# Kernel optimization log

Hardware: AMD Instinct MI355X
Metric: run time of the kernel (lower is better)

Reference implementation:

```python
import jax, jax.numpy as jnp
import numpy as np

B, H, W, C = 32, 56, 56, 256
HEADS, WS, SS, MLP = 8, 7, 3, 1024
N = WS * WS          # tokens per window = 49
HD = C // HEADS      # head dim = 32
SCALE = HD ** -0.5
EPS = 1e-5


def _rel_pos_index():
    coords = np.stack(np.meshgrid(np.arange(WS), np.arange(WS), indexing='ij')).reshape(2, -1)
    rel = (coords[:, :, None] - coords[:, None, :]).transpose(1, 2, 0)
    rel[:, :, 0] += WS - 1
    rel[:, :, 1] += WS - 1
    rel[:, :, 0] *= 2 * WS - 1
    return rel.sum(-1)  # (49, 49) int


def _shift_mask():
    ma = np.zeros((H, W), np.float32)
    sl = (slice(0, -WS), slice(-WS, -SS), slice(-SS, None))
    cnt = 0
    for hs in sl:
        for ws_ in sl:
            ma[hs, ws_] = cnt
            cnt += 1
    mw = ma.reshape(H // WS, WS, W // WS, WS).transpose(0, 2, 1, 3).reshape(-1, N)
    diff = mw[:, None, :] - mw[:, :, None]
    return np.where(diff != 0, np.float32(-100.0), np.float32(0.0))  # (nW, 49, 49)


_RPI = _rel_pos_index()
_MASK = jnp.asarray(_shift_mask())


def _ln(x, g, b):
    mu = jnp.mean(x, -1, keepdims=True)
    var = jnp.mean(jnp.square(x - mu), -1, keepdims=True)
    return (x - mu) * jax.lax.rsqrt(var + EPS) * g + b


def setup_inputs() -> dict:
    key = jax.random.key(0)
    ks = jax.random.split(key, 6)
    s = 0.02
    return {
        'x': jax.random.normal(ks[0], (B, H * W, C), jnp.float32),
        'qkv_w': jax.random.normal(ks[1], (C, 3 * C), jnp.float32) * s,
        'qkv_b': jnp.zeros((3 * C,), jnp.float32),
        'proj_w': jax.random.normal(ks[2], (C, C), jnp.float32) * s,
        'proj_b': jnp.zeros((C,), jnp.float32),
        'rel_bias': jax.random.normal(ks[3], ((2 * WS - 1) ** 2, HEADS), jnp.float32) * s,
        'ln1_g': jnp.ones((C,), jnp.float32),
        'ln1_b': jnp.zeros((C,), jnp.float32),
        'ln2_g': jnp.ones((C,), jnp.float32),
        'ln2_b': jnp.zeros((C,), jnp.float32),
        'mlp_w1': jax.random.normal(ks[4], (C, MLP), jnp.float32) * s,
        'mlp_b1': jnp.zeros((MLP,), jnp.float32),
        'mlp_w2': jax.random.normal(ks[5], (MLP, C), jnp.float32) * s,
        'mlp_b2': jnp.zeros((C,), jnp.float32),
    }


def reference(x, qkv_w, qkv_b, proj_w, proj_b, rel_bias,
              ln1_g, ln1_b, ln2_g, ln2_b, mlp_w1, mlp_b1, mlp_w2, mlp_b2):
    b = x.shape[0]
    nW = (H // WS) * (W // WS)

    x_skip = x
    xn = _ln(x, ln1_g, ln1_b).reshape(b, H, W, C)
    shifted = jnp.roll(xn, (-SS, -SS), axis=(1, 2))
    # window partition -> (b*nW, N, C)
    xw = shifted.reshape(b, H // WS, WS, W // WS, WS, C)
    xw = xw.transpose(0, 1, 3, 2, 4, 5).reshape(-1, N, C)

    qkv = (xw @ qkv_w + qkv_b).reshape(-1, N, 3, HEADS, HD).transpose(2, 0, 3, 1, 4)
    q, k, v = qkv[0] * SCALE, qkv[1], qkv[2]  # (b*nW, heads, N, hd)

    attn = jnp.einsum('bhnd,bhmd->bhnm', q, k)
    bias = rel_bias[_RPI.reshape(-1)].reshape(N, N, HEADS).transpose(2, 0, 1)
    attn = attn + bias[None]
    attn = attn.reshape(b, nW, HEADS, N, N) + _MASK[None, :, None]
    attn = jax.nn.softmax(attn.reshape(-1, HEADS, N, N), axis=-1)

    out = jnp.einsum('bhnm,bhmd->bhnd', attn, v)
    out = out.transpose(0, 2, 1, 3).reshape(-1, N, C)
    out = out @ proj_w + proj_b

    # window reverse -> (b, H, W, C)
    out = out.reshape(b, H // WS, W // WS, WS, WS, C)
    out = out.transpose(0, 1, 3, 2, 4, 5).reshape(b, H, W, C)
    out = jnp.roll(out, (SS, SS), axis=(1, 2)).reshape(b, H * W, C)

    x = x_skip + out
    x_skip2 = x
    xn2 = _ln(x, ln2_g, ln2_b)
    h = jax.nn.gelu(xn2 @ mlp_w1 + mlp_b1, approximate=False)
    h = h @ mlp_w2 + mlp_b2
    return x_skip2 + h
```

## Files before the change

### kernel.cpp

```cpp
#include <hip/hip_runtime.h>


typedef unsigned short u16;
typedef __attribute__((ext_vector_type(8))) short bfrag8;
typedef __attribute__((ext_vector_type(8))) unsigned short u16x8;
typedef __attribute__((ext_vector_type(4))) float f32x4;

#define WS_TOK 49
#define C_DIM 256
#define M_ROWS 100352
#define N_WIN 2048
#define SCALE_Q 0.17677669529663689f

#if defined(__has_builtin)
#  if __has_builtin(__builtin_amdgcn_global_load_lds)
#    define HAVE_GLL 1
#  endif
#endif
#ifndef HAVE_GLL
#  define HAVE_GLL 0
#endif

__device__ __forceinline__ float u2f(u16 u) {
    union { unsigned int i; float f; } c; c.i = ((unsigned int)u) << 16; return c.f;
}
__device__ __forceinline__ u16 f2u(float f) {
    union { float f; unsigned int i; } c; c.f = f;
    unsigned int i = c.i;
    return (u16)((i + 0x7fffu + ((i >> 16) & 1u)) >> 16);
}
__device__ __forceinline__ int regionOf(int h) {
    return h < 49 ? 0 : (h < 53 ? 1 : 2);
}
__device__ __forceinline__ float gelu_tanh(float v) {
    const float y = 0.79788456080286536f * (v + 0.044715f * v * v * v);
    const float e = __expf(2.f * y);
    const float t = 1.f - 2.f / (e + 1.f);
    return 0.5f * v * (1.f + t);
}

__device__ __forceinline__ void g2l16(const u16* g, u16* l) {
#if HAVE_GLL
    __builtin_amdgcn_global_load_lds((const __attribute__((address_space(1))) void*)g,
                                     (__attribute__((address_space(3))) void*)l, 16, 0, 0);
#else
    *(bfrag8*)l = *(const bfrag8*)g;
#endif
}

__global__ void transpose_k(const float* __restrict__ in, u16* __restrict__ out,
                            int R, int Ccols) {
    int i = blockIdx.x * 256 + threadIdx.x;
    if (i < R * Ccols) {
        int r = i / Ccols, c = i - r * Ccols;
        out[(size_t)c * R + r] = f2u(in[i]);
    }
}

__global__ __launch_bounds__(256) void ln_kernel(const float* __restrict__ xin,
                                                 const float* __restrict__ g,
                                                 const float* __restrict__ b,
                                                 u16* __restrict__ out, int mode) {
    const int w = threadIdx.x >> 6, lane = threadIdx.x & 63;
    const int r = blockIdx.x * 4 + w;
    int s = r;
    if (mode == 0) {
        const int win = r / WS_TOK, tok = r - win * WS_TOK;
        const int b_ = win >> 6, w64 = win & 63;
        const int wr = w64 >> 3, wc = w64 & 7;
        const int th = tok / 7, tw = tok - th * 7;
        int hh = wr * 7 + th + 3; if (hh >= 56) hh -= 56;
        int ww = wc * 7 + tw + 3; if (ww >= 56) ww -= 56;
        s = b_ * 3136 + hh * 56 + ww;
    }
    const float4 u = *(const float4*)(xin + (size_t)s * C_DIM + lane * 4);
    float f0 = u.x, f1 = u.y, f2 = u.z, f3 = u.w;
    float s1 = f0 + f1 + f2 + f3;
    float s2 = f0 * f0 + f1 * f1 + f2 * f2 + f3 * f3;
#pragma unroll
    for (int off = 32; off; off >>= 1) {
        s1 += __shfl_xor(s1, off, 64);
        s2 += __shfl_xor(s2, off, 64);
    }
    const float mu = s1 * (1.f / 256.f);
    const float rs = rsqrtf(s2 * (1.f / 256.f) - mu * mu + 1e-5f);
    const float4 ug = *(const float4*)(g + lane * 4);
    const float4 ub = *(const float4*)(b + lane * 4);
    ushort4 o;
    o.x = f2u((f0 - mu) * rs * ug.x + ub.x);
    o.y = f2u((f1 - mu) * rs * ug.y + ub.y);
    o.z = f2u((f2 - mu) * rs * ug.z + ub.z);
    o.w = f2u((f3 - mu) * rs * ug.w + ub.w);
    *(ushort4*)(out + (size_t)r * C_DIM + lane * 4) = o;
}

template <int KD, int ND, int NY, int EPI>
__global__ __launch_bounds__(256) void gemm_bt(const u16* __restrict__ A,
                                               const u16* __restrict__ Bt,
                                               const float* __restrict__ bias,
                                               u16* __restrict__ o0,
                                               u16* __restrict__ o1,
                                               u16* __restrict__ o2,
                                               float* __restrict__ fo,
                                               const float* __restrict__ res) {
    __shared__ __align__(16) char pool[17408];
    u16* As = (u16*)pool;
    u16* Bs = (u16*)(pool + 8192);
    const int tid = threadIdx.x;
    const int bid = blockIdx.x;
    const int m0 = (bid / NY) * 128;
    const int n0 = (bid % NY) * 128;
    const int wid = tid >> 6, lane = tid & 63;
    const int wy = wid >> 1, wx = wid & 1;
    const int l15 = lane & 15, lsel = lane >> 4;

    f32x4 acc[4][4] = {};
    const u16* Ag = A + (size_t)m0 * KD;
    const u16* Bg = Bt + (size_t)n0 * KD;

    for (int k0 = 0; k0 < KD; k0 += 32) {
#pragma unroll
        for (int p = 0; p < 2; ++p) {
            const int idx = p * 256 + tid;
            const int row = idx >> 2, ks = (idx & 3) << 3;
            g2l16(Ag + (size_t)row * KD + k0 + ks, As + idx * 8);
            g2l16(Bg + (size_t)row * KD + k0 + ks, Bs + idx * 8);
        }
        __syncthreads();
        bfrag8 af[4], bfv[4];
#pragma unroll
        for (int m = 0; m < 4; ++m)
            af[m] = *(const bfrag8*)(As + (wy * 64 + m * 16 + l15) * 32 + lsel * 8);
#pragma unroll
        for (int n = 0; n < 4; ++n)
            bfv[n] = *(const bfrag8*)(Bs + (wx * 64 + n * 16 + l15) * 32 + lsel * 8);
#pragma unroll
        for (int m = 0; m < 4; ++m)
#pragma unroll
            for (int n = 0; n < 4; ++n)
                acc[m][n] = __builtin_amdgcn_mfma_f32_16x16x32_bf16(af[m], bfv[n],
                                                                    acc[m][n], 0, 0, 0);
        __syncthreads();
    }

    float* Ts = (float*)pool + wid * (16 * 68);
    const int r  = lane >> 2;
    const int cg = (lane & 3) << 4;

#pragma unroll
    for (int m = 0; m < 4; ++m) {
#pragma unroll
        for (int n = 0; n < 4; ++n)
#pragma unroll
            for (int reg = 0; reg < 4; ++reg)
                Ts[(lsel * 4 + reg) * 68 + n * 16 + l15] = acc[m][n][reg];
        float vals[16];
#pragma unroll
        for (int j = 0; j < 4; ++j)
            *(f32x4*)(vals + 4 * j) = *(const f32x4*)(Ts + r * 68 + cg + 4 * j);

        const int gr  = m0 + wy * 64 + m * 16 + r;
        const int gc0 = n0 + wx * 64 + cg;
        float bias16[16];
#pragma unroll
        for (int j = 0; j < 4; ++j)
            *(f32x4*)(bias16 + 4 * j) = *(const f32x4*)(bias + gc0 + 4 * j);

        if (EPI == 0) {
            const int win = gr / WS_TOK, tok = gr - win * WS_TOK;
            const int part = gc0 >> 8, head = (gc0 >> 5) & 7, hd = gc0 & 31;
            u16* dst = (part == 0) ? o0 : (part == 1) ? o1 : o2;
            const float sc = (part == 0) ? SCALE_Q : 1.f;
            const size_t di = (size_t)win * 8 * (WS_TOK * 32) + (size_t)tok * 32 +
                              (size_t)head * (WS_TOK * 32) + hd;
            u16x8 pk[2];
#pragma unroll
            for (int j = 0; j < 16; ++j)
                ((u16*)pk)[j] = f2u((vals[j] + bias16[j]) * sc);
            *(u16x8*)(dst + di)     = pk[0];
            *(u16x8*)(dst + di + 8) = pk[1];
        } else if (EPI == 1) {
            const int win = gr / WS_TOK, tok = gr - win * WS_TOK;
            const int b_ = win >> 6, w64 = win & 63;
            const int wr = w64 >> 3, wc = w64 & 7;
            const int th = tok / 7, tw = tok - th * 7;
            int hh = wr * 7 + th + 3; if (hh >= 56) hh -= 56;
            int ww = wc * 7 + tw + 3; if (ww >= 56) ww -= 56;
            const size_t di = ((size_t)b_ * 3136 + hh * 56 + ww) * C_DIM + gc0;
#pragma unroll
            for (int j = 0; j < 4; ++j) {
                f32x4 rr = *(const f32x4*)(res + di + 4 * j);
                f32x4 o;
#pragma unroll
                for (int e = 0; e < 4; ++e)
                    o[e] = rr[e] + vals[4 * j + e] + bias16[4 * j + e];
                *(f32x4*)(fo + di + 4 * j) = o;
            }
        } else if (EPI == 2) {
            u16x8 pk[2];
#pragma unroll
            for (int j = 0; j < 16; ++j)
                ((u16*)pk)[j] = f2u(gelu_tanh(vals[j] + bias16[j]));
            u16* dst = o0 + (size_t)gr * ND + gc0;
            *(u16x8*)dst       = pk[0];
            *(u16x8*)(dst + 8) = pk[1];
        } else {
            const size_t di = (size_t)gr * ND + gc0;
#pragma unroll
            for (int j = 0; j < 4; ++j) {
                f32x4 rr = *(const f32x4*)(res + di + 4 * j);
                f32x4 o;
#pragma unroll
                for (int e = 0; e < 4; ++e)
                    o[e] = rr[e] + vals[4 * j + e] + bias16[4 * j + e];
                *(f32x4*)(fo + di + 4 * j) = o;
            }
        }
    }
}

__device__ __forceinline__ void stage_w1t(const u16* __restrict__ w1T, u16* dst,
                                          int kc, int k0, int tid) {
#pragma unroll
    for (int p = 0; p < 4; ++p) {
        const int i = p * 256 + tid;
        const int row = i >> 3, s = i & 7;
        g2l16(w1T + (size_t)(kc * 128 + row) * 256 + k0 + ((s ^ (row & 7)) << 3),
              dst + i * 8);
    }
}
__device__ __forceinline__ void stage_w2t(const u16* __restrict__ w2T, u16* dst,
                                          int kc, int bs, int tid) {
#pragma unroll
    for (int p = 0; p < 4; ++p) {
        const int i = p * 256 + tid;
        const int row = i >> 2, s = i & 3;
        g2l16(w2T + (size_t)row * 1024 + kc * 128 + bs * 32 +
                  ((s ^ ((row >> 1) & 3)) << 3),
              dst + i * 8);
    }
}

__global__ __launch_bounds__(256, 2) void fused_mlp(const u16* __restrict__ z,
                                                    const u16* __restrict__ w1T,
                                                    const float* __restrict__ b1,
                                                    const u16* __restrict__ w2T,
                                                    const float* __restrict__ b2,
                                                    float* __restrict__ out) {
    __shared__ __align__(16) u16 pool[40960];
    u16* zS  = pool;
    u16* wb0 = pool + 16384;
    u16* wb1 = pool + 24576;
    u16* hc  = pool + 32768;
    const int tid = threadIdx.x;
    const int wid = tid >> 6, lane = tid & 63;
    const int wy = wid >> 1, wx = wid & 1;
    const int l15 = lane & 15, lsel = lane >> 4;
    const int m0 = blockIdx.x * 64;

#pragma unroll
    for (int p = 0; p < 8; ++p) {
        const int i = p * 256 + tid;
        const int row = i >> 5, s = i & 31;
        g2l16(z + (size_t)(m0 + row) * 256 + ((s ^ (row & 7)) << 3), zS + i * 8);
    }
    stage_w1t(w1T, wb0, 0, 0, tid);
    __syncthreads();

    f32x4 acc2[2][8] = {};

    for (int kc = 0; kc < 8; ++kc) {
        float b1v[4];
#pragma unroll
        for (int n = 0; n < 4; ++n)
            b1v[n] = b1[kc * 128 + wx * 64 + n * 16 + l15];

        f32x4 acc1[2][4] = {};
#pragma unroll
        for (int ks = 0; ks < 4; ++ks) {
            u16* wc = (ks & 1) ? wb1 : wb0;
            u16* wn = (ks & 1) ? wb0 : wb1;
            if (ks < 3) stage_w1t(w1T, wn, kc, (ks + 1) * 64, tid);
            else        stage_w2t(w2T, wn, kc, 0, tid);
#pragma unroll
            for (int sub = 0; sub < 2; ++sub) {
                bfrag8 af[2], bf[4];
#pragma unroll
                for (int m = 0; m < 2; ++m) {
                    const int r = wy * 32 + m * 16 + l15;
                    af[m] = *(const bfrag8*)(zS + r * 256 +
                             ((ks * 64 + sub * 32 + lsel * 8) ^ ((r & 7) << 3)));
                }
#pragma unroll
                for (int n = 0; n < 4; ++n) {
                    const int r = wx * 64 + n * 16 + l15;
                    bf[n] = *(const bfrag8*)(wc + r * 64 +
                             ((sub * 32 + lsel * 8) ^ ((r & 7) << 3)));
                }
#pragma unroll
                for (int m = 0; m < 2; ++m)
#pragma unroll
                    for (int n = 0; n < 4; ++n)
                        acc1[m][n] = __builtin_amdgcn_mfma_f32_16x16x32_bf16(
                            af[m], bf[n], acc1[m][n], 0, 0, 0);
            }
            if (ks == 3) {
#pragma unroll
                for (int m = 0; m < 2; ++m)
#pragma unroll
                    for (int n = 0; n < 4; ++n)
#pragma unroll
                        for (int reg = 0; reg < 4; ++reg) {
                            const int rh = wy * 32 + m * 16 + lsel * 4 + reg;
                            const int ch = wx * 64 + n * 16 + l15;
                            hc[rh * 128 + (ch ^ ((rh & 15) << 3))] =
                                f2u(gelu_tanh(acc1[m][n][reg] + b1v[n]));
                        }
            }
            __syncthreads();
        }
#pragma unroll
        for (int bs = 0; bs < 4; ++bs) {
            u16* wc = (bs & 1) ? wb1 : wb0;
            u16* wn = (bs & 1) ? wb0 : wb1;
            if (bs < 3)      stage_w2t(w2T, wn, kc, bs + 1, tid);
            else if (kc < 7) stage_w1t(w1T, wn, kc + 1, 0, tid);
            bfrag8 a2[2], bb[8];
#pragma unroll
            for (int m = 0; m < 2; ++m) {
                const int r = wy * 32 + m * 16 + l15;
                a2[m] = *(const bfrag8*)(hc + r * 128 +
                         ((bs * 32 + lsel * 8) ^ ((r & 15) << 3)));
            }
#pragma unroll
            for (int n = 0; n < 8; ++n) {
                const int r = wx * 128 + n * 16 + l15;
                bb[n] = *(const bfrag8*)(wc + r * 32 +
                         ((lsel * 8) ^ (((r >> 1) & 3) << 3)));
            }
#pragma unroll
            for (int m = 0; m < 2; ++m)
#pragma unroll
                for (int n = 0; n < 8; ++n)
                    acc2[m][n] = __builtin_amdgcn_mfma_f32_16x16x32_bf16(
                        a2[m], bb[n], acc2[m][n], 0, 0, 0);
            __syncthreads();
        }
    }

    float b2v[8];
#pragma unroll
    for (int n = 0; n < 8; ++n)
        b2v[n] = b2[wx * 128 + n * 16 + l15];
#pragma unroll
    for (int m = 0; m < 2; ++m)
#pragma unroll
        for (int reg = 0; reg < 4; ++reg) {
            const int row = m0 + wy * 32 + m * 16 + lsel * 4 + reg;
#pragma unroll
            for (int n = 0; n < 8; ++n) {
                const size_t di = (size_t)row * 256 + wx * 128 + n * 16 + l15;
                out[di] += acc2[m][n][reg] + b2v[n];
            }
        }
}

__global__ __launch_bounds__(256) void attn_kernel(const u16* __restrict__ q,
                                                   const u16* __restrict__ k,
                                                   const u16* __restrict__ v,
                                                   const float* __restrict__ relb,
                                                   u16* __restrict__ ao) {
    __shared__ __align__(16) u16 PbAll[4][64 * 64];
    __shared__ __align__(16) u16 VtAll[4][32 * 64];
    const int wid = threadIdx.x >> 6;
    const int lane = threadIdx.x & 63;
    u16* Pb = PbAll[wid];
    u16* Vt = VtAll[wid];
    const int bid = blockIdx.x * 4 + wid;
    const int head = bid & 7, win = bid >> 3;
    const int w64 = win & 63;
    const int wr = w64 >> 3, wc = w64 & 7;
    const int l15 = lane & 15, lsel = lane >> 4;
    const size_t base = (size_t)bid * (WS_TOK * 32);
    const u16* qb = q + base;
    const u16* kb = k + base;
    const u16* vb = v + base;

    for (int idx = lane; idx < WS_TOK * 32; idx += 64) {
        const int tok = idx >> 5, dim = idx & 31;
        Vt[dim * 64 + tok] = vb[idx];
    }
    for (int i = lane; i < 32 * 15; i += 64) {
        const int dim = i / 15, tok = 49 + (i - dim * 15);
        Vt[dim * 64 + tok] = 0;
    }

    bfrag8 qf[4], kf[4];
#pragma unroll
    for (int m = 0; m < 4; ++m) {
        int tok = m * 16 + l15; if (tok > 48) tok = 48;
        qf[m] = *(const bfrag8*)(qb + tok * 32 + lsel * 8);
    }
#pragma unroll
    for (int n = 0; n < 4; ++n) {
        int tok = n * 16 + l15; if (tok > 48) tok = 48;
        kf[n] = *(const bfrag8*)(kb + tok * 32 + lsel * 8);
    }
    f32x4 S[4][4] = {};
#pragma unroll
    for (int m = 0; m < 4; ++m)
#pragma unroll
        for (int n = 0; n < 4; ++n)
            S[m][n] = __builtin_amdgcn_mfma_f32_16x16x32_bf16(qf[m], kf[n], S[m][n], 0, 0, 0);

#pragma unroll
    for (int m = 0; m < 4; ++m) {
#pragma unroll
        for (int reg = 0; reg < 4; ++reg) {
            const int row = m * 16 + lsel * 4 + reg;
            const int rowc = row > 48 ? 48 : row;
            const int ih = rowc / 7, iw = rowc - ih * 7;
            const int ri = regionOf(wr * 7 + ih) * 3 + regionOf(wc * 7 + iw);
            float sv[4];
#pragma unroll
            for (int n = 0; n < 4; ++n) {
                const int col = n * 16 + l15;
                float val = S[m][n][reg];
                if (col > 48) {
                    val = -1e30f;
                } else {
                    const int jh = col / 7, jw = col - jh * 7;
                    val += relb[((ih - jh + 6) * 13 + (iw - jw + 6)) * 8 + head];
                    const int rj = regionOf(wr * 7 + jh) * 3 + regionOf(wc * 7 + jw);
                    if (ri != rj) val -= 100.f;
                }
                sv[n] = val;
            }
            float mx = fmaxf(fmaxf(sv[0], sv[1]), fmaxf(sv[2], sv[3]));
#pragma unroll
            for (int off = 1; off < 16; off <<= 1) mx = fmaxf(mx, __shfl_xor(mx, off, 64));
            float p[4], sum = 0.f;
#pragma unroll
            for (int n = 0; n < 4; ++n) { p[n] = __expf(sv[n] - mx); sum += p[n]; }
#pragma unroll
            for (int off = 1; off < 16; off <<= 1) sum += __shfl_xor(sum, off, 64);
            const float inv = 1.f / sum;
#pragma unroll
            for (int n = 0; n < 4; ++n)
                Pb[row * 64 + n * 16 + l15] = f2u(p[n] * inv);
        }
    }

    f32x4 O[4][2] = {};
    bfrag8 vf[2][2];
#pragma unroll
    for (int n = 0; n < 2; ++n) {
        vf[n][0] = *(const bfrag8*)(Vt + (n * 16 + l15) * 64 + lsel * 8);
        vf[n][1] = *(const bfrag8*)(Vt + (n * 16 + l15) * 64 + 32 + lsel * 8);
    }
#pragma unroll
    for (int m = 0; m < 4; ++m) {
        const bfrag8 pf0 = *(const bfrag8*)(Pb + (m * 16 + l15) * 64 + lsel * 8);
        const bfrag8 pf1 = *(const bfrag8*)(Pb + (m * 16 + l15) * 64 + 32 + lsel * 8);
#pragma unroll
        for (int n = 0; n < 2; ++n) {
            O[m][n] = __builtin_amdgcn_mfma_f32_16x16x32_bf16(pf0, vf[n][0], O[m][n], 0, 0, 0);
            O[m][n] = __builtin_amdgcn_mfma_f32_16x16x32_bf16(pf1, vf[n][1], O[m][n], 0, 0, 0);
        }
    }
    const size_t aob = (size_t)win * (WS_TOK * C_DIM) + head * 32;
#pragma unroll
    for (int m = 0; m < 4; ++m) {
#pragma unroll
        for (int reg = 0; reg < 4; ++reg) {
            const int row = m * 16 + lsel * 4 + reg;
            if (row < WS_TOK) {
#pragma unroll
                for (int n = 0; n < 2; ++n)
                    ao[aob + (size_t)row * C_DIM + n * 16 + l15] = f2u(O[m][n][reg]);
            }
        }
    }
}

extern "C" void kernel_launch(void* const* d_in, const int* in_sizes, int n_in,
                              void* d_out, int out_size, void* d_ws, size_t ws_size,
                              hipStream_t stream) {
    (void)in_sizes; (void)n_in; (void)out_size; (void)ws_size;
    const float* x      = (const float*)d_in[0];
    const float* qkv_w  = (const float*)d_in[1];
    const float* qkv_b  = (const float*)d_in[2];
    const float* proj_w = (const float*)d_in[3];
    const float* proj_b = (const float*)d_in[4];
    const float* relb   = (const float*)d_in[5];
    const float* ln1g   = (const float*)d_in[6];
    const float* ln1b   = (const float*)d_in[7];
    const float* ln2g   = (const float*)d_in[8];
    const float* ln2b   = (const float*)d_in[9];
    const float* w1     = (const float*)d_in[10];
    const float* b1     = (const float*)d_in[11];
    const float* w2     = (const float*)d_in[12];
    const float* b2     = (const float*)d_in[13];
    float* out = (float*)d_out;

    const size_t SZ = (size_t)M_ROWS * C_DIM;
    u16* wsu  = (u16*)d_ws;
    u16* xw   = wsu;
    u16* qq   = wsu + SZ;
    u16* kk   = wsu + 2 * SZ;
    u16* vv   = wsu + 3 * SZ;
    u16* ao   = wsu + 4 * SZ;
    u16* z    = xw;
    u16* qkvT = wsu + 5 * SZ;
    u16* projT = qkvT + 256 * 768;
    u16* w1T  = projT + 256 * 256;
    u16* w2T  = w1T + 256 * 1024;

    transpose_k<<<768, 256, 0, stream>>>(qkv_w, qkvT, 256, 768);
    transpose_k<<<256, 256, 0, stream>>>(proj_w, projT, 256, 256);
    transpose_k<<<1024, 256, 0, stream>>>(w1, w1T, 256, 1024);
    transpose_k<<<1024, 256, 0, stream>>>(w2, w2T, 1024, 256);

    ln_kernel<<<M_ROWS / 4, 256, 0, stream>>>(x, ln1g, ln1b, xw, 0);

    gemm_bt<256, 768, 6, 0><<<784 * 6, 256, 0, stream>>>(xw, qkvT, qkv_b,
                                                         qq, kk, vv, nullptr, nullptr);

    attn_kernel<<<N_WIN * 8 / 4, 256, 0, stream>>>(qq, kk, vv, relb, ao);

    gemm_bt<256, 256, 2, 1><<<784 * 2, 256, 0, stream>>>(ao, projT, proj_b,
                                                         nullptr, nullptr, nullptr, out, x);

    ln_kernel<<<M_ROWS / 4, 256, 0, stream>>>(out, ln2g, ln2b, z, 1);

    fused_mlp<<<M_ROWS / 64, 256, 0, stream>>>(z, w1T, b1, w2T, b2, out);
}
```

Baseline: 717.4 us.

## Pipeline fused MLP with manual waitcnt barriers, cheaper GELU, vectorized epilogue

Replaces __syncthreads in the fused MLP kernel with explicit s_waitcnt vmcnt(4) plus s_barrier, so the next weight tile's async global-to-LDS loads can stay in flight while the current tile is computed. It also hoists all LDS fragment loads ahead of the MFMA chain and raises wave priority around the MFMAs. GELU is rewritten as v*sigmoid(...) using an fma, exp and hardware reciprocal. The final residual add now goes through an LDS transpose so global reads and writes use float4 vectors. The hand-counted vmcnt values and the LDS reuse in the epilogue risk races if the outstanding-load counts are wrong.

```diff
diff --git a/kernel.cpp b/kernel.cpp
--- a/kernel.cpp
+++ b/kernel.cpp
@@ -32,11 +32,11 @@
 __device__ __forceinline__ int regionOf(int h) {
     return h < 49 ? 0 : (h < 53 ? 1 : 2);
 }
-__device__ __forceinline__ float gelu_tanh(float v) {
-    const float y = 0.79788456080286536f * (v + 0.044715f * v * v * v);
-    const float e = __expf(2.f * y);
-    const float t = 1.f - 2.f / (e + 1.f);
-    return 0.5f * v * (1.f + t);
+__device__ __forceinline__ float gelu_fast(float v) {
+    const float v2 = v * v;
+    const float u = v * __builtin_fmaf(-0.0713548162f, v2, -1.5957691216f);
+    const float e = __expf(u);
+    return v * __builtin_amdgcn_rcpf(1.f + e);
 }
 
 __device__ __forceinline__ void g2l16(const u16* g, u16* l) {
@@ -200,7 +200,7 @@
             u16x8 pk[2];
 #pragma unroll
             for (int j = 0; j < 16; ++j)
-                ((u16*)pk)[j] = f2u(gelu_tanh(vals[j] + bias16[j]));
+                ((u16*)pk)[j] = f2u(gelu_fast(vals[j] + bias16[j]));
             u16* dst = o0 + (size_t)gr * ND + gc0;
             *(u16x8*)dst       = pk[0];
             *(u16x8*)(dst + 8) = pk[1];
@@ -265,7 +265,6 @@
         g2l16(z + (size_t)(m0 + row) * 256 + ((s ^ (row & 7)) << 3), zS + i * 8);
     }
     stage_w1t(w1T, wb0, 0, 0, tid);
-    __syncthreads();
 
     f32x4 acc2[2][8] = {};
 
@@ -274,6 +273,7 @@
 #pragma unroll
         for (int n = 0; n < 4; ++n)
             b1v[n] = b1[kc * 128 + wx * 64 + n * 16 + l15];
+        asm volatile("" ::: "memory");
 
         f32x4 acc1[2][4] = {};
 #pragma unroll
@@ -282,28 +282,49 @@
             u16* wn = (ks & 1) ? wb0 : wb1;
             if (ks < 3) stage_w1t(w1T, wn, kc, (ks + 1) * 64, tid);
             else        stage_w2t(w2T, wn, kc, 0, tid);
-#pragma unroll
-            for (int sub = 0; sub < 2; ++sub) {
-                bfrag8 af[2], bf[4];
-#pragma unroll
-                for (int m = 0; m < 2; ++m) {
-                    const int r = wy * 32 + m * 16 + l15;
-                    af[m] = *(const bfrag8*)(zS + r * 256 +
-                             ((ks * 64 + sub * 32 + lsel * 8) ^ ((r & 7) << 3)));
-                }
-#pragma unroll
-                for (int n = 0; n < 4; ++n) {
-                    const int r = wx * 64 + n * 16 + l15;
-                    bf[n] = *(const bfrag8*)(wc + r * 64 +
-                             ((sub * 32 + lsel * 8) ^ ((r & 7) << 3)));
-                }
-#pragma unroll
-                for (int m = 0; m < 2; ++m)
-#pragma unroll
-                    for (int n = 0; n < 4; ++n)
-                        acc1[m][n] = __builtin_amdgcn_mfma_f32_16x16x32_bf16(
-                            af[m], bf[n], acc1[m][n], 0, 0, 0);
-            }
+            asm volatile("s_waitcnt vmcnt(4)" ::: "memory");
+            __builtin_amdgcn_sched_barrier(0);
+            __builtin_amdgcn_s_barrier();
+            bfrag8 af[2], bf[4];
+#pragma unroll
+            for (int m = 0; m < 2; ++m) {
+                const int r = wy * 32 + m * 16 + l15;
+                af[m] = *(const bfrag8*)(zS + r * 256 +
+                         ((ks * 64 + lsel * 8) ^ ((r & 7) << 3)));
+            }
+#pragma unroll
+            for (int n = 0; n < 4; ++n) {
+                const int r = wx * 64 + n * 16 + l15;
+                bf[n] = *(const bfrag8*)(wc + r * 64 +
+                         ((lsel * 8) ^ ((r & 7) << 3)));
+            }
+            bfrag8 af2[2], bf2[4];
+#pragma unroll
+            for (int m = 0; m < 2; ++m) {
+                const int r = wy * 32 + m * 16 + l15;
+                af2[m] = *(const bfrag8*)(zS + r * 256 +
+                          ((ks * 64 + 32 + lsel * 8) ^ ((r & 7) << 3)));
+            }
+#pragma unroll
+            for (int n = 0; n < 4; ++n) {
+                const int r = wx * 64 + n * 16 + l15;
+                bf2[n] = *(const bfrag8*)(wc + r * 64 +
+                          ((32 + lsel * 8) ^ ((r & 7) << 3)));
+            }
+            __builtin_amdgcn_s_setprio(1);
+#pragma unroll
+            for (int m = 0; m < 2; ++m)
+#pragma unroll
+                for (int n = 0; n < 4; ++n)
+                    acc1[m][n] = __builtin_amdgcn_mfma_f32_16x16x32_bf16(
+                        af[m], bf[n], acc1[m][n], 0, 0, 0);
+#pragma unroll
+            for (int m = 0; m < 2; ++m)
+#pragma unroll
+                for (int n = 0; n < 4; ++n)
+                    acc1[m][n] = __builtin_amdgcn_mfma_f32_16x16x32_bf16(
+                        af2[m], bf2[n], acc1[m][n], 0, 0, 0);
+            __builtin_amdgcn_s_setprio(0);
             if (ks == 3) {
 #pragma unroll
                 for (int m = 0; m < 2; ++m)
@@ -314,10 +335,12 @@
                             const int rh = wy * 32 + m * 16 + lsel * 4 + reg;
                             const int ch = wx * 64 + n * 16 + l15;
                             hc[rh * 128 + (ch ^ ((rh & 15) << 3))] =
-                                f2u(gelu_tanh(acc1[m][n][reg] + b1v[n]));
+                                f2u(gelu_fast(acc1[m][n][reg] + b1v[n]));
                         }
-            }
-            __syncthreads();
+                asm volatile("s_waitcnt lgkmcnt(0)" ::: "memory");
+                __builtin_amdgcn_sched_barrier(0);
+            }
+            __builtin_amdgcn_s_barrier();
         }
 #pragma unroll
         for (int bs = 0; bs < 4; ++bs) {
@@ -325,6 +348,10 @@
             u16* wn = (bs & 1) ? wb0 : wb1;
             if (bs < 3)      stage_w2t(w2T, wn, kc, bs + 1, tid);
             else if (kc < 7) stage_w1t(w1T, wn, kc + 1, 0, tid);
+            if (bs == 3 && kc == 7) asm volatile("s_waitcnt vmcnt(0)" ::: "memory");
+            else                    asm volatile("s_waitcnt vmcnt(4)" ::: "memory");
+            __builtin_amdgcn_sched_barrier(0);
+            __builtin_amdgcn_s_barrier();
             bfrag8 a2[2], bb[8];
 #pragma unroll
             for (int m = 0; m < 2; ++m) {
@@ -338,31 +365,46 @@
                 bb[n] = *(const bfrag8*)(wc + r * 32 +
                          ((lsel * 8) ^ (((r >> 1) & 3) << 3)));
             }
+            __builtin_amdgcn_s_setprio(1);
 #pragma unroll
             for (int m = 0; m < 2; ++m)
 #pragma unroll
                 for (int n = 0; n < 8; ++n)
                     acc2[m][n] = __builtin_amdgcn_mfma_f32_16x16x32_bf16(
                         a2[m], bb[n], acc2[m][n], 0, 0, 0);
-            __syncthreads();
-        }
-    }
-
-    float b2v[8];
-#pragma unroll
-    for (int n = 0; n < 8; ++n)
-        b2v[n] = b2[wx * 128 + n * 16 + l15];
-#pragma unroll
-    for (int m = 0; m < 2; ++m)
-#pragma unroll
-        for (int reg = 0; reg < 4; ++reg) {
-            const int row = m0 + wy * 32 + m * 16 + lsel * 4 + reg;
-#pragma unroll
-            for (int n = 0; n < 8; ++n) {
-                const size_t di = (size_t)row * 256 + wx * 128 + n * 16 + l15;
-                out[di] += acc2[m][n][reg] + b2v[n];
-            }
-        }
+            __builtin_amdgcn_s_setprio(0);
+            __builtin_amdgcn_s_barrier();
+        }
+    }
+
+    float* Ts = (float*)pool + wid * (16 * 132);
+    const int r  = lane >> 2;
+    const int cg = (lane & 3) << 5;
+#pragma unroll
+    for (int m = 0; m < 2; ++m) {
+#pragma unroll
+        for (int n = 0; n < 8; ++n)
+#pragma unroll
+            for (int reg = 0; reg < 4; ++reg)
+                Ts[(lsel * 4 + reg) * 132 + n * 16 + l15] = acc2[m][n][reg];
+        float vals[32];
+#pragma unroll
+        for (int j = 0; j < 8; ++j)
+            *(f32x4*)(vals + 4 * j) = *(const f32x4*)(Ts + r * 132 + cg + 4 * j);
+
+        const int gr = m0 + wy * 32 + m * 16 + r;
+        const size_t dbase = (size_t)gr * 256 + wx * 128 + cg;
+#pragma unroll
+        for (int j = 0; j < 8; ++j) {
+            f32x4 rr = *(const f32x4*)(out + dbase + 4 * j);
+            f32x4 bb4 = *(const f32x4*)(b2 + wx * 128 + cg + 4 * j);
+            f32x4 o;
+#pragma unroll
+            for (int e = 0; e < 4; ++e)
+                o[e] = rr[e] + vals[4 * j + e] + bb4[e];
+            *(f32x4*)(out + dbase + 4 * j) = o;
+        }
+    }
 }
 
 __global__ __launch_bounds__(256) void attn_kernel(const u16* __restrict__ q,
```

New measurement: 724.3 us. About the same (+1.0%).

## Double GEMM K-tile and XOR-swizzle shared memory to cut bank conflicts

Applied to the files above, without the earlier changes.

The GEMM kernel now stages 64-wide K slices instead of 32, which halves the number of barrier pairs per K loop. Its shared-memory tiles use an XOR swizzle on 16-byte chunks keyed by row, so the MFMA fragment reads avoid bank conflicts. The attention kernel applies the same swizzle to the transposed V and probability buffers. The cost is twice the GEMM shared memory (32 KB), which may lower occupancy.

```diff
diff --git a/kernel.cpp b/kernel.cpp
--- a/kernel.cpp
+++ b/kernel.cpp
@@ -103,9 +103,9 @@
                                                u16* __restrict__ o2,
                                                float* __restrict__ fo,
                                                const float* __restrict__ res) {
-    __shared__ __align__(16) char pool[17408];
+    __shared__ __align__(16) char pool[32768];
     u16* As = (u16*)pool;
-    u16* Bs = (u16*)(pool + 8192);
+    u16* Bs = (u16*)(pool + 16384);
     const int tid = threadIdx.x;
     const int bid = blockIdx.x;
     const int m0 = (bid / NY) * 128;
@@ -118,28 +118,38 @@
     const u16* Ag = A + (size_t)m0 * KD;
     const u16* Bg = Bt + (size_t)n0 * KD;
 
-    for (int k0 = 0; k0 < KD; k0 += 32) {
-#pragma unroll
-        for (int p = 0; p < 2; ++p) {
+    for (int k0 = 0; k0 < KD; k0 += 64) {
+#pragma unroll
+        for (int p = 0; p < 4; ++p) {
             const int idx = p * 256 + tid;
-            const int row = idx >> 2, ks = (idx & 3) << 3;
-            g2l16(Ag + (size_t)row * KD + k0 + ks, As + idx * 8);
-            g2l16(Bg + (size_t)row * KD + k0 + ks, Bs + idx * 8);
+            const int row = idx >> 3, s = idx & 7;
+            const int so = (s ^ (row & 7)) << 3;
+            g2l16(Ag + (size_t)row * KD + k0 + so, As + idx * 8);
+            g2l16(Bg + (size_t)row * KD + k0 + so, Bs + idx * 8);
         }
         __syncthreads();
-        bfrag8 af[4], bfv[4];
-#pragma unroll
-        for (int m = 0; m < 4; ++m)
-            af[m] = *(const bfrag8*)(As + (wy * 64 + m * 16 + l15) * 32 + lsel * 8);
-#pragma unroll
-        for (int n = 0; n < 4; ++n)
-            bfv[n] = *(const bfrag8*)(Bs + (wx * 64 + n * 16 + l15) * 32 + lsel * 8);
-#pragma unroll
-        for (int m = 0; m < 4; ++m)
-#pragma unroll
-            for (int n = 0; n < 4; ++n)
-                acc[m][n] = __builtin_amdgcn_mfma_f32_16x16x32_bf16(af[m], bfv[n],
-                                                                    acc[m][n], 0, 0, 0);
+#pragma unroll
+        for (int kh = 0; kh < 2; ++kh) {
+            bfrag8 af[4], bfv[4];
+#pragma unroll
+            for (int m = 0; m < 4; ++m) {
+                const int r = wy * 64 + m * 16 + l15;
+                af[m] = *(const bfrag8*)(As + r * 64 +
+                         ((kh * 32 + lsel * 8) ^ ((r & 7) << 3)));
+            }
+#pragma unroll
+            for (int n = 0; n < 4; ++n) {
+                const int r = wx * 64 + n * 16 + l15;
+                bfv[n] = *(const bfrag8*)(Bs + r * 64 +
+                          ((kh * 32 + lsel * 8) ^ ((r & 7) << 3)));
+            }
+#pragma unroll
+            for (int m = 0; m < 4; ++m)
+#pragma unroll
+                for (int n = 0; n < 4; ++n)
+                    acc[m][n] = __builtin_amdgcn_mfma_f32_16x16x32_bf16(
+                        af[m], bfv[n], acc[m][n], 0, 0, 0);
+        }
         __syncthreads();
     }
 
@@ -388,11 +398,11 @@
 
     for (int idx = lane; idx < WS_TOK * 32; idx += 64) {
         const int tok = idx >> 5, dim = idx & 31;
-        Vt[dim * 64 + tok] = vb[idx];
+        Vt[dim * 64 + (tok ^ ((dim & 7) << 3))] = vb[idx];
     }
     for (int i = lane; i < 32 * 15; i += 64) {
         const int dim = i / 15, tok = 49 + (i - dim * 15);
-        Vt[dim * 64 + tok] = 0;
+        Vt[dim * 64 + (tok ^ ((dim & 7) << 3))] = 0;
     }
 
     bfrag8 qf[4], kf[4];
@@ -447,7 +457,7 @@
             const float inv = 1.f / sum;
 #pragma unroll
             for (int n = 0; n < 4; ++n)
-                Pb[row * 64 + n * 16 + l15] = f2u(p[n] * inv);
+                Pb[row * 64 + ((n * 16 + l15) ^ ((row & 7) << 3))] = f2u(p[n] * inv);
         }
     }
 
@@ -455,13 +465,17 @@
     bfrag8 vf[2][2];
 #pragma unroll
     for (int n = 0; n < 2; ++n) {
-        vf[n][0] = *(const bfrag8*)(Vt + (n * 16 + l15) * 64 + lsel * 8);
-        vf[n][1] = *(const bfrag8*)(Vt + (n * 16 + l15) * 64 + 32 + lsel * 8);
+        const int r = n * 16 + l15;
+        vf[n][0] = *(const bfrag8*)(Vt + r * 64 + ((lsel * 8) ^ ((r & 7) << 3)));
+        vf[n][1] = *(const bfrag8*)(Vt + r * 64 + ((32 + lsel * 8) ^ ((r & 7) << 3)));
     }
 #pragma unroll
     for (int m = 0; m < 4; ++m) {
-        const bfrag8 pf0 = *(const bfrag8*)(Pb + (m * 16 + l15) * 64 + lsel * 8);
-        const bfrag8 pf1 = *(const bfrag8*)(Pb + (m * 16 + l15) * 64 + 32 + lsel * 8);
+        const int r = m * 16 + l15;
+        const bfrag8 pf0 = *(const bfrag8*)(Pb + r * 64 +
+                            ((lsel * 8) ^ ((r & 7) << 3)));
+        const bfrag8 pf1 = *(const bfrag8*)(Pb + r * 64 +
+                            ((32 + lsel * 8) ^ ((r & 7) << 3)));
 #pragma unroll
         for (int n = 0; n < 2; ++n) {
             O[m][n] = __builtin_amdgcn_mfma_f32_16x16x32_bf16(pf0, vf[n][0], O[m][n], 0, 0, 0);
```

Result: faster. 674.2 us (-6.0%).
